# Performance work log

Hardware: AMD Instinct MI355X
Metric: run time of the kernel (lower is better)

Reference implementation:

```python
import jax, jax.numpy as jnp
import numpy as np

VOCAB = 50257
EMBED = 256
OUT = 5
B = 512
S = 512

def setup_inputs() -> dict:
    key = jax.random.key(0)
    k1, k2, k3, k4, k5, k6 = jax.random.split(key, 6)
    input_x = jax.random.randint(k1, (B, S), 0, VOCAB, dtype=jnp.int64 if jax.config.jax_enable_x64 else jnp.int32)
    lengths = jax.random.randint(k2, (B,), 1, S + 1, dtype=jnp.int32)  # true ragged lengths in [1, S]
    input_y = jax.random.randint(k3, (B,), 0, OUT, dtype=jnp.int32)
    emb = jax.random.normal(k4, (VOCAB, EMBED), dtype=jnp.float32)
    W = jax.random.normal(k5, (OUT, EMBED), dtype=jnp.float32) * (1.0 / np.sqrt(EMBED))
    b = jax.random.normal(k6, (OUT,), dtype=jnp.float32) * 0.01
    return {"input_x": input_x, "lengths": lengths, "input_y": input_y, "emb": emb, "W": W, "b": b}

def reference(input_x, lengths, input_y, emb, W, b):
    # Embedding gather: [B, S, E]
    x = emb[input_x]
    # Ragged mean pooling via mask (replaces the per-sample Python loop)
    mask = (jnp.arange(S)[None, :] < lengths[:, None]).astype(x.dtype)  # [B, S]
    pooled = jnp.einsum('bse,bs->be', x, mask) / lengths[:, None].astype(x.dtype)  # [B, E]
    # Linear + log-softmax
    logits = pooled @ W.T + b  # [B, O]
    logp = jax.nn.log_softmax(logits, axis=-1)
    # NLLLoss (mean reduction)
    loss = -jnp.take_along_axis(logp, input_y[:, None].astype(jnp.int32), axis=1).mean()
    return loss
```

## Files before the change

kernel.cpp:

```cpp
#include <hip/hip_runtime.h>

#define VOCAB 50257
#define EMBED 256
#define OUT 5
#define BATCH 512
#define SEQ 512

__global__ __launch_bounds__(256) void k_embw(const float* __restrict__ emb,
                                              const float* __restrict__ W,
                                              float* __restrict__ embW) {
    __shared__ float sW[OUT * EMBED];
    for (int i = threadIdx.x; i < OUT * EMBED; i += 256) sW[i] = W[i];
    __syncthreads();

    const int wave = threadIdx.x >> 6;
    const int lane = threadIdx.x & 63;
    const int v = blockIdx.x * 4 + wave;
    if (v >= VOCAB) return;

    const float4 e = *(const float4*)(emb + (size_t)v * EMBED + lane * 4);

    float p[OUT];
#pragma unroll
    for (int o = 0; o < OUT; ++o) {
        const float4 w = *(const float4*)(sW + o * EMBED + lane * 4);
        p[o] = e.x * w.x + e.y * w.y + e.z * w.z + e.w * w.w;
    }

#pragma unroll
    for (int o = 0; o < OUT; ++o) {
        float val = p[o];
#pragma unroll
        for (int off = 32; off > 0; off >>= 1)
            val += __shfl_down(val, off, 64);
        if (lane == 0) embW[(size_t)v * OUT + o] = val;
    }
}

__global__ __launch_bounds__(256) void k_pool(const int* __restrict__ x,
                                              const int* __restrict__ lengths,
                                              const int* __restrict__ y,
                                              const float* __restrict__ bias,
                                              const float* __restrict__ embW,
                                              float* __restrict__ losses) {
    const int b = blockIdx.x;
    const int len = lengths[b];
    const int* xb = x + (size_t)b * SEQ;

    float acc[OUT] = {0.f, 0.f, 0.f, 0.f, 0.f};
    for (int s = threadIdx.x; s < len; s += 256) {
        const int tok = xb[s];
        const float* r = embW + (size_t)tok * OUT;
#pragma unroll
        for (int o = 0; o < OUT; ++o) acc[o] += r[o];
    }

#pragma unroll
    for (int o = 0; o < OUT; ++o) {
#pragma unroll
        for (int off = 32; off > 0; off >>= 1)
            acc[o] += __shfl_down(acc[o], off, 64);
    }

    __shared__ float red[4][OUT];
    const int wave = threadIdx.x >> 6;
    const int lane = threadIdx.x & 63;
    if (lane == 0) {
#pragma unroll
        for (int o = 0; o < OUT; ++o) red[wave][o] = acc[o];
    }
    __syncthreads();

    if (threadIdx.x == 0) {
        float logits[OUT];
        const float inv = 1.0f / (float)len;
#pragma unroll
        for (int o = 0; o < OUT; ++o)
            logits[o] = (red[0][o] + red[1][o] + red[2][o] + red[3][o]) * inv + bias[o];

        float m = logits[0];
#pragma unroll
        for (int o = 1; o < OUT; ++o) m = fmaxf(m, logits[o]);
        float sum = 0.f;
#pragma unroll
        for (int o = 0; o < OUT; ++o) sum += __expf(logits[o] - m);
        const float lse = m + __logf(sum);
        losses[b] = lse - logits[y[b]];
    }
}

__global__ __launch_bounds__(256) void k_reduce(const float* __restrict__ losses,
                                                float* __restrict__ out) {
    float v = losses[threadIdx.x] + losses[threadIdx.x + 256];
#pragma unroll
    for (int off = 32; off > 0; off >>= 1)
        v += __shfl_down(v, off, 64);
    __shared__ float red[4];
    if ((threadIdx.x & 63) == 0) red[threadIdx.x >> 6] = v;
    __syncthreads();
    if (threadIdx.x == 0)
        out[0] = (red[0] + red[1] + red[2] + red[3]) * (1.0f / (float)BATCH);
}

extern "C" void kernel_launch(void* const* d_in, const int* in_sizes, int n_in,
                              void* d_out, int out_size, void* d_ws, size_t ws_size,
                              hipStream_t stream) {
    const int*   x       = (const int*)d_in[0];
    const int*   lengths = (const int*)d_in[1];
    const int*   y       = (const int*)d_in[2];
    const float* emb     = (const float*)d_in[3];
    const float* W       = (const float*)d_in[4];
    const float* bias    = (const float*)d_in[5];

    float* embW   = (float*)d_ws;
    float* losses = embW + (size_t)VOCAB * OUT;

    k_embw<<<(VOCAB + 3) / 4, 256, 0, stream>>>(emb, W, embW);
    k_pool<<<BATCH, 256, 0, stream>>>(x, lengths, y, bias, embW, losses);
    k_reduce<<<1, 256, 0, stream>>>(losses, (float*)d_out);
}
```

Before: 114.8 us.

## Use grid-stride embW projection, padded rows, and atomic loss reduction

```diff
diff --git a/kernel.cpp b/kernel.cpp
--- a/kernel.cpp
+++ b/kernel.cpp
@@ -3,6 +3,7 @@
 #define VOCAB 50257
 #define EMBED 256
 #define OUT 5
+#define ROWSTRIDE 8
 #define BATCH 512
 #define SEQ 512
 
@@ -13,27 +14,33 @@
     for (int i = threadIdx.x; i < OUT * EMBED; i += 256) sW[i] = W[i];
     __syncthreads();
 
-    const int wave = threadIdx.x >> 6;
-    const int lane = threadIdx.x & 63;
-    const int v = blockIdx.x * 4 + wave;
-    if (v >= VOCAB) return;
+    const int lane   = threadIdx.x & 63;
+    const int waveId = blockIdx.x * 4 + (threadIdx.x >> 6);
+    const int nWaves = gridDim.x * 4;
 
-    const float4 e = *(const float4*)(emb + (size_t)v * EMBED + lane * 4);
+    float4 w[OUT];
+#pragma unroll
+    for (int o = 0; o < OUT; ++o)
+        w[o] = *(const float4*)(sW + o * EMBED + lane * 4);
 
-    float p[OUT];
+    for (int v = waveId; v < VOCAB; v += nWaves) {
+        const float4 e = *(const float4*)(emb + (size_t)v * EMBED + lane * 4);
+        float p[OUT];
 #pragma unroll
-    for (int o = 0; o < OUT; ++o) {
-        const float4 w = *(const float4*)(sW + o * EMBED + lane * 4);
-        p[o] = e.x * w.x + e.y * w.y + e.z * w.z + e.w * w.w;
-    }
+        for (int o = 0; o < OUT; ++o)
+            p[o] = e.x * w[o].x + e.y * w[o].y + e.z * w[o].z + e.w * w[o].w;
 
 #pragma unroll
-    for (int o = 0; o < OUT; ++o) {
-        float val = p[o];
+        for (int o = 0; o < OUT; ++o) {
 #pragma unroll
-        for (int off = 32; off > 0; off >>= 1)
-            val += __shfl_down(val, off, 64);
-        if (lane == 0) embW[(size_t)v * OUT + o] = val;
+            for (int off = 32; off > 0; off >>= 1)
+                p[o] += __shfl_down(p[o], off, 64);
+        }
+        if (lane == 0) {
+            float* r = embW + (size_t)v * ROWSTRIDE;
+#pragma unroll
+            for (int o = 0; o < OUT; ++o) r[o] = p[o];
+        }
     }
 }
 
@@ -42,17 +49,18 @@
                                               const int* __restrict__ y,
                                               const float* __restrict__ bias,
                                               const float* __restrict__ embW,
-                                              float* __restrict__ losses) {
+                                              float* __restrict__ out) {
     const int b = blockIdx.x;
     const int len = lengths[b];
     const int* xb = x + (size_t)b * SEQ;
 
     float acc[OUT] = {0.f, 0.f, 0.f, 0.f, 0.f};
     for (int s = threadIdx.x; s < len; s += 256) {
-        const int tok = xb[s];
-        const float* r = embW + (size_t)tok * OUT;
-#pragma unroll
-        for (int o = 0; o < OUT; ++o) acc[o] += r[o];
+        const float* r = embW + (size_t)xb[s] * ROWSTRIDE;
+        const float4 r0 = *(const float4*)(r);
+        const float  r4 = r[4];
+        acc[0] += r0.x; acc[1] += r0.y; acc[2] += r0.z; acc[3] += r0.w;
+        acc[4] += r4;
     }
 
 #pragma unroll
@@ -85,21 +93,9 @@
 #pragma unroll
         for (int o = 0; o < OUT; ++o) sum += __expf(logits[o] - m);
         const float lse = m + __logf(sum);
-        losses[b] = lse - logits[y[b]];
+        const float loss = lse - logits[y[b]];
+        atomicAdd(out, loss * (1.0f / (float)BATCH));
     }
-}
-
-__global__ __launch_bounds__(256) void k_reduce(const float* __restrict__ losses,
-                                                float* __restrict__ out) {
-    float v = losses[threadIdx.x] + losses[threadIdx.x + 256];
-#pragma unroll
-    for (int off = 32; off > 0; off >>= 1)
-        v += __shfl_down(v, off, 64);
-    __shared__ float red[4];
-    if ((threadIdx.x & 63) == 0) red[threadIdx.x >> 6] = v;
-    __syncthreads();
-    if (threadIdx.x == 0)
-        out[0] = (red[0] + red[1] + red[2] + red[3]) * (1.0f / (float)BATCH);
 }
 
 extern "C" void kernel_launch(void* const* d_in, const int* in_sizes, int n_in,
@@ -112,10 +108,10 @@
     const float* W       = (const float*)d_in[4];
     const float* bias    = (const float*)d_in[5];
 
-    float* embW   = (float*)d_ws;
-    float* losses = embW + (size_t)VOCAB * OUT;
+    float* embW = (float*)d_ws;
 
-    k_embw<<<(VOCAB + 3) / 4, 256, 0, stream>>>(emb, W, embW);
-    k_pool<<<BATCH, 256, 0, stream>>>(x, lengths, y, bias, embW, losses);
-    k_reduce<<<1, 256, 0, stream>>>(losses, (float*)d_out);
+    hipMemsetAsync(d_out, 0, sizeof(float), stream);
+
+    k_embw<<<2048, 256, 0, stream>>>(emb, W, embW);
+    k_pool<<<BATCH, 256, 0, stream>>>(x, lengths, y, bias, embW, (float*)d_out);
 }
```

New measurement: 116.5 us. No clear change (+1.5%).
